# Kernel tuning notes

Hardware: AMD Instinct MI355X
Metric: run time of the kernel (lower is better)

The kernel has to match this reference:

```python
import jax, jax.numpy as jnp
import numpy as np

B, C, H, W = 16, 256, 32, 32
LN_EPS = 1e-5


def setup_inputs() -> dict:
    key = jax.random.key(0)
    ks = jax.random.split(key, 12)
    s = 1.0 / np.sqrt(C)
    x = jax.random.normal(ks[0], (B, C, H, W), dtype=jnp.float32)
    # Linear weights stored as [in, out] (torch stores [out, in]; math is x @ W_in_out + b)
    wq = jax.random.uniform(ks[1], (C, C), jnp.float32, -s, s)
    bq = jax.random.uniform(ks[2], (C,), jnp.float32, -s, s)
    wk = jax.random.uniform(ks[3], (C, C), jnp.float32, -s, s)
    bk = jax.random.uniform(ks[4], (C,), jnp.float32, -s, s)
    wv = jax.random.uniform(ks[5], (C, C), jnp.float32, -s, s)
    bv = jax.random.uniform(ks[6], (C,), jnp.float32, -s, s)
    w1 = jax.random.uniform(ks[7], (C, C), jnp.float32, -s, s)
    b1 = jax.random.uniform(ks[8], (C,), jnp.float32, -s, s)
    w2 = jax.random.uniform(ks[9], (C, C), jnp.float32, -s, s)
    b2 = jax.random.uniform(ks[10], (C,), jnp.float32, -s, s)
    gamma = jnp.ones((C,), jnp.float32)
    beta = jnp.zeros((C,), jnp.float32)
    return {"x": x, "wq": wq, "bq": bq, "wk": wk, "bk": bk, "wv": wv, "bv": bv,
            "w1": w1, "b1": b1, "w2": w2, "b2": b2, "gamma": gamma, "beta": beta}


def reference(x, wq, bq, wk, bk, wv, bv, w1, b1, w2, b2, gamma, beta):
    Bd, Cd, Hd, Wd = x.shape
    t = x.reshape(Bd, Cd, Hd * Wd).transpose(0, 2, 1)  # [B, N, C]
    q = t @ wq + bq
    k = t @ wk + bk
    v = t @ wv + bv
    # matrix[b,i,j] = q[b,i,:] . k[b,j,:]  (no 1/sqrt(d) scaling, as in source)
    m = jnp.einsum('bic,bjc->bij', q, k)
    # softmax over dim=-2 (the query axis i)
    m = jax.nn.softmax(m, axis=-2)
    # att[b,j,c] = sum_i v[b,i,c] * m[b,i,j]  (v^T @ m, then permute)
    att = jnp.einsum('bic,bij->bjc', v, m)  # [B, N, C]
    # MLP (SiLU, hidden = C), dropout p=0 -> identity; DropPath eval -> identity
    att = jax.nn.silu(att @ w1 + b1) @ w2 + b2
    # LayerNorm over channel dim
    mu = jnp.mean(att, axis=-1, keepdims=True)
    var = jnp.var(att, axis=-1, keepdims=True)
    att = (att - mu) * jax.lax.rsqrt(var + LN_EPS) * gamma + beta
    return att.transpose(0, 2, 1).reshape(Bd, Cd, Hd, Wd)
```

## Files before the change

### kernel.cpp

```cpp
#include <hip/hip_runtime.h>

#define BB 16
#define CC 256
#define NN 1024

typedef _Float16 f16;
typedef __attribute__((ext_vector_type(8))) _Float16 half8;
typedef __attribute__((ext_vector_type(4))) float f32x4;

__device__ __forceinline__ half8 ldg8(const f16* p) {
  return *reinterpret_cast<const half8*>(p);
}

__device__ __forceinline__ void gll16(const f16* g, f16* l) {
  __builtin_amdgcn_global_load_lds((const __attribute__((address_space(1))) void*)g,
                                   (__attribute__((address_space(3))) void*)l, 16, 0, 0);
}

#define VMCNT(n) asm volatile("s_waitcnt vmcnt(" #n ")" ::: "memory")
#define BAR() __builtin_amdgcn_s_barrier()

__device__ __forceinline__ void stage32k8(const f16* __restrict__ g, f16* l, int wave, int lane) {
#pragma unroll
  for (int k = 0; k < 4; ++k) {
    int ob = k * 4096 + wave * 512;
    gll16(g + ob + lane * 8, l + ob);
  }
}

struct WP5 {
  const float* s[5];
  f16* d[5];
};

__global__ void __launch_bounds__(256) k_packW(WP5 p) {
  __shared__ float ws[256][17];
  int m = blockIdx.y, ct = blockIdx.x;
  const float* W = p.s[m];
  f16* wp = p.d[m];
  int tid = threadIdx.x;
  int col = tid & 15, cig = tid >> 4;
#pragma unroll
  for (int pg = 0; pg < 16; ++pg) {
    int ci = pg * 16 + cig;
    ws[ci][col] = W[(size_t)ci * 256 + ct * 16 + col];
  }
  __syncthreads();
  int lane = tid & 63, wave = tid >> 6;
  int row16 = lane & 15, quad = lane >> 4;
#pragma unroll
  for (int kk = 0; kk < 2; ++kk) {
    int kc = wave * 2 + kk;
    half8 o;
#pragma unroll
    for (int j = 0; j < 8; ++j) o[j] = (f16)ws[kc * 32 + quad * 8 + j][row16];
    *reinterpret_cast<half8*>(wp + ((size_t)ct * 8 + kc) * 512 + lane * 8) = o;
  }
}

struct QkvSmem {
  union {
    struct { f16 hi[32][264]; f16 lo[32][264]; } ts;
    f16 ex[2][16][264];
    f16 exv[256][40];
  };
};

__global__ void __launch_bounds__(256) k_qkv(const float* __restrict__ x,
    const f16* __restrict__ wqp, const f16* __restrict__ wkp, const f16* __restrict__ wvp,
    const float* __restrict__ bq, const float* __restrict__ bk, const float* __restrict__ bv,
    f16* __restrict__ qp, f16* __restrict__ kp, f16* __restrict__ vp, int b_base) {
  __shared__ QkvSmem sm;
  int bl = blockIdx.x, bg = b_base + bl, n0 = blockIdx.y * 32;
  int tid = threadIdx.x, wave = tid >> 6, lane = tid & 63;
  int row16 = lane & 15, quad = lane >> 4;
  int g = wave >> 1, h = wave & 1;

#pragma unroll
  for (int e = tid; e < 2048; e += 256) {
    int c = e >> 3, n4 = (e & 7) << 2;
    float4 u = *reinterpret_cast<const float4*>(x + (size_t)(bg * CC + c) * NN + n0 + n4);
    float uv[4] = {u.x, u.y, u.z, u.w};
#pragma unroll
    for (int i = 0; i < 4; ++i) {
      f16 hh = (f16)uv[i];
      sm.ts.hi[n4 + i][c] = hh;
      sm.ts.lo[n4 + i][c] = (f16)(uv[i] - (float)hh);
    }
  }
  __syncthreads();

  half8 ah[8], al[8];
#pragma unroll
  for (int kc = 0; kc < 8; ++kc) {
    ah[kc] = *reinterpret_cast<const half8*>(&sm.ts.hi[g * 16 + row16][kc * 32 + quad * 8]);
    al[kc] = *reinterpret_cast<const half8*>(&sm.ts.lo[g * 16 + row16][kc * 32 + quad * 8]);
  }
  __syncthreads();

  const f16* WTs[2]    = {wqp, wkp};
  const float* biases[2] = {bq, bk};
  f16* outs[2]         = {qp, kp};
#pragma unroll
  for (int z = 0; z < 2; ++z) {
    const f16* WT = WTs[z];
    const float* bias = biases[z];
    f16* outp = outs[z];
#pragma unroll
    for (int cp = 0; cp < 2; ++cp) {
      f32x4 acch[4], accl[4];
#pragma unroll
      for (int u = 0; u < 4; ++u) { acch[u] = {0.f,0.f,0.f,0.f}; accl[u] = {0.f,0.f,0.f,0.f}; }
#pragma unroll
      for (int kc = 0; kc < 8; ++kc) {
#pragma unroll
        for (int u = 0; u < 4; ++u) {
          int ct = h * 8 + cp * 4 + u;
          half8 b = ldg8(WT + ((size_t)ct * 8 + kc) * 512 + lane * 8);
          acch[u] = __builtin_amdgcn_mfma_f32_16x16x32_f16(ah[kc], b, acch[u], 0, 0, 0);
          accl[u] = __builtin_amdgcn_mfma_f32_16x16x32_f16(al[kc], b, accl[u], 0, 0, 0);
        }
      }
#pragma unroll
      for (int u = 0; u < 4; ++u) {
        int ct = h * 8 + cp * 4 + u;
        int co = ct * 16 + row16;
        float bb = bias[co];
#pragma unroll
        for (int r = 0; r < 4; ++r)
          sm.ex[g][quad * 4 + r][co] = (f16)(acch[u][r] + accl[u][r] + bb);
      }
    }
    const f16* exr = &sm.ex[g][row16][0];
    size_t fb = ((size_t)bl * 64 + (n0 >> 4) + g) * 8;
#pragma unroll
    for (int k = 0; k < 4; ++k) {
      int kc = h * 4 + k;
      half8 hv = *reinterpret_cast<const half8*>(exr + kc * 32 + quad * 8);
      *reinterpret_cast<half8*>(outp + (fb + kc) * 512 + lane * 8) = hv;
    }
  }
  __syncthreads();

#pragma unroll
  for (int cp = 0; cp < 2; ++cp) {
    f32x4 acch[4], accl[4];
#pragma unroll
    for (int u = 0; u < 4; ++u) { acch[u] = {0.f,0.f,0.f,0.f}; accl[u] = {0.f,0.f,0.f,0.f}; }
#pragma unroll
    for (int kc = 0; kc < 8; ++kc) {
#pragma unroll
      for (int u = 0; u < 4; ++u) {
        int ct = h * 8 + cp * 4 + u;
        half8 b = ldg8(wvp + ((size_t)ct * 8 + kc) * 512 + lane * 8);
        acch[u] = __builtin_amdgcn_mfma_f32_16x16x32_f16(ah[kc], b, acch[u], 0, 0, 0);
        accl[u] = __builtin_amdgcn_mfma_f32_16x16x32_f16(al[kc], b, accl[u], 0, 0, 0);
      }
    }
#pragma unroll
    for (int u = 0; u < 4; ++u) {
      int ct = h * 8 + cp * 4 + u;
      int co = ct * 16 + row16;
      float bb = bv[co];
#pragma unroll
      for (int r = 0; r < 4; ++r)
        sm.exv[co][g * 16 + quad * 4 + r] = (f16)(acch[u][r] + accl[u][r] + bb);
    }
  }
  __syncthreads();
  size_t vb = ((size_t)bl * 32 + blockIdx.y) * 16;
#pragma unroll
  for (int f = 0; f < 4; ++f) {
    int ct = wave * 4 + f;
    half8 o = *reinterpret_cast<const half8*>(&sm.exv[ct * 16 + row16][quad * 8]);
    *reinterpret_cast<half8*>(vp + (vb + ct) * 512 + lane * 8) = o;
  }
}

struct AttnSmem {
  union {
    struct {
      f16 QB[64 * 256];
      f16 VB[64 * 256];
    } s;
    struct {
      float Ocmb[4][16][132];
      f16 ex[4][16][264];
    } e;
  } u;
  f16 P[8][16][40];
  float ml[8][2][16];
  float lnbuf[8][2][16];
};

__global__ void __launch_bounds__(512, 2) k_attn_mlp(
    const f16* __restrict__ qp, const f16* __restrict__ kp, const f16* __restrict__ vp,
    const f16* __restrict__ w1p, const float* __restrict__ b1,
    const f16* __restrict__ w2p, const float* __restrict__ b2,
    const float* __restrict__ gamma, const float* __restrict__ beta,
    float* __restrict__ out, int b_base) {
  __shared__ AttnSmem sm;
  int bl = blockIdx.x, bg = b_base + bl;
  int j0 = blockIdx.y * 64;
  int tid = threadIdx.x, wave = tid >> 6, lane = tid & 63;
  int row16 = lane & 15, quad = lane >> 4;
  int jt_l = wave & 3, p = wave >> 2;
  int jw = j0 + jt_l * 16;

  const f16* kbase = kp + (size_t)bl * NN * CC;
  int jt = (j0 >> 4) + jt_l;
  half8 kf[8];
#pragma unroll
  for (int kc = 0; kc < 8; ++kc)
    kf[kc] = ldg8(kbase + ((size_t)jt * 8 + kc) * 512 + lane * 8);

  const f16* qbase = qp + (size_t)bl * NN * CC;
  const f16* vbase = vp + (size_t)bl * CC * NN;

  stage32k8(qbase, sm.u.s.QB, wave, lane);
  stage32k8(vbase, sm.u.s.VB, wave, lane);
  VMCNT(4);
  BAR();

  f32x4 O[16];
#pragma unroll
  for (int ct = 0; ct < 16; ++ct) O[ct] = {0.f, 0.f, 0.f, 0.f};
  float m_run[4], l_lane[4];
#pragma unroll
  for (int r = 0; r < 4; ++r) { m_run[r] = -1e30f; l_lane[r] = 0.f; }

  const f16* QBp = &sm.u.s.QB[p * 8192];
  const f16* VBp = &sm.u.s.VB[p * 8192];

  for (int it = 0; it < 16; ++it) {
    f32x4 s[2];
#pragma unroll
    for (int f = 0; f < 2; ++f) s[f] = {0.f, 0.f, 0.f, 0.f};
#pragma unroll
    for (int kc = 0; kc < 8; ++kc) {
#pragma unroll
      for (int f = 0; f < 2; ++f) {
        half8 b = *reinterpret_cast<const half8*>(&QBp[(f * 8 + kc) * 512 + lane * 8]);
        s[f] = __builtin_amdgcn_mfma_f32_16x16x32_f16(kf[kc], b, s[f], 0, 0, 0);
      }
    }
    BAR();
    stage32k8(qbase + (size_t)((it + 1) & 15) * 16384, sm.u.s.QB, wave, lane);

    float alpha[4];
#pragma unroll
    for (int r = 0; r < 4; ++r) {
      float mx = fmaxf(s[0][r], s[1][r]);
#pragma unroll
      for (int off = 1; off < 16; off <<= 1) mx = fmaxf(mx, __shfl_xor(mx, off, 64));
      float mnew = fmaxf(m_run[r], mx);
      alpha[r] = __expf(m_run[r] - mnew);
      m_run[r] = mnew;
      float ps = 0.f;
#pragma unroll
      for (int f = 0; f < 2; ++f) {
        float pv = __expf(s[f][r] - mnew);
        ps += pv;
        sm.P[wave][quad * 4 + r][f * 16 + row16] = (f16)pv;
      }
      l_lane[r] = l_lane[r] * alpha[r] + ps;
    }
#pragma unroll
    for (int ct = 0; ct < 16; ++ct)
#pragma unroll
      for (int r = 0; r < 4; ++r) O[ct][r] *= alpha[r];

    VMCNT(4);
    BAR();

    {
      half8 pf = *reinterpret_cast<const half8*>(&sm.P[wave][row16][quad * 8]);
#pragma unroll
      for (int ct = 0; ct < 16; ++ct) {
        half8 vf = *reinterpret_cast<const half8*>(&VBp[ct * 512 + lane * 8]);
        O[ct] = __builtin_amdgcn_mfma_f32_16x16x32_f16(pf, vf, O[ct], 0, 0, 0);
      }
    }
    BAR();
    stage32k8(vbase + (size_t)((it + 1) & 15) * 16384, sm.u.s.VB, wave, lane);
    VMCNT(4);
    BAR();
  }
  VMCNT(0);
  BAR();

#pragma unroll
  for (int r = 0; r < 4; ++r) {
#pragma unroll
    for (int off = 1; off < 16; off <<= 1) l_lane[r] += __shfl_xor(l_lane[r], off, 64);
  }
  if (row16 == 0) {
#pragma unroll
    for (int r = 0; r < 4; ++r) {
      sm.ml[wave][0][quad * 4 + r] = m_run[r];
      sm.ml[wave][1][quad * 4 + r] = l_lane[r];
    }
  }
  BAR();

  int partner = wave ^ 4;
  float aS[4], invL[4];
#pragma unroll
  for (int r = 0; r < 4; ++r) {
    int j = quad * 4 + r;
    float ma = m_run[r], mb = sm.ml[partner][0][j];
    float M = fmaxf(ma, mb);
    float L = l_lane[r] * __expf(ma - M) + sm.ml[partner][1][j] * __expf(mb - M);
    aS[r] = __expf(ma - M);
    invL[r] = 1.f / L;
  }
#pragma unroll
  for (int ct = 0; ct < 16; ++ct)
#pragma unroll
    for (int r = 0; r < 4; ++r) O[ct][r] *= aS[r];

  if (p == 0) {
#pragma unroll
    for (int ct = 0; ct < 8; ++ct)
#pragma unroll
      for (int r = 0; r < 4; ++r)
        sm.u.e.Ocmb[jt_l][quad * 4 + r][ct * 16 + row16] = O[ct][r];
  }
  BAR();
  if (p == 1) {
#pragma unroll
    for (int ct = 0; ct < 8; ++ct)
#pragma unroll
      for (int r = 0; r < 4; ++r) {
        float v = sm.u.e.Ocmb[jt_l][quad * 4 + r][ct * 16 + row16] + O[ct][r];
        sm.u.e.ex[jt_l][quad * 4 + r][ct * 16 + row16] = (f16)(v * invL[r]);
      }
  }
  BAR();
  if (p == 0) {
#pragma unroll
    for (int ct = 8; ct < 16; ++ct)
#pragma unroll
      for (int r = 0; r < 4; ++r)
        sm.u.e.Ocmb[jt_l][quad * 4 + r][(ct - 8) * 16 + row16] = O[ct][r];
  }
  BAR();
  if (p == 1) {
#pragma unroll
    for (int ct = 8; ct < 16; ++ct)
#pragma unroll
      for (int r = 0; r < 4; ++r) {
        float v = sm.u.e.Ocmb[jt_l][quad * 4 + r][(ct - 8) * 16 + row16] + O[ct][r];
        sm.u.e.ex[jt_l][quad * 4 + r][ct * 16 + row16] = (f16)(v * invL[r]);
      }
  }
  BAR();

  half8 af[8];
#pragma unroll
  for (int kc = 0; kc < 8; ++kc)
    af[kc] = *reinterpret_cast<const half8*>(&sm.u.e.ex[jt_l][row16][kc * 32 + quad * 8]);

  f16* ex2 = reinterpret_cast<f16*>(&sm.u.e.Ocmb[0][0][0]);

#pragma unroll
  for (int q8 = 0; q8 < 8; ++q8) {
    int ct = p * 8 + q8;
    f32x4 acc = {0.f, 0.f, 0.f, 0.f};
    const f16* brow = w1p + ((size_t)ct * 8) * 512 + lane * 8;
#pragma unroll
    for (int kc = 0; kc < 8; ++kc)
      acc = __builtin_amdgcn_mfma_f32_16x16x32_f16(af[kc], ldg8(brow + kc * 512), acc, 0, 0, 0);
    int co = ct * 16 + row16;
    float bb = b1[co];
#pragma unroll
    for (int r = 0; r < 4; ++r) {
      float xg = acc[r] + bb;
      float hh = xg / (1.f + __expf(-xg));
      ex2[((size_t)jt_l * 16 + quad * 4 + r) * 264 + co] = (f16)hh;
    }
  }
  BAR();

  half8 hf[8];
#pragma unroll
  for (int kc = 0; kc < 8; ++kc)
    hf[kc] = *reinterpret_cast<const half8*>(&ex2[((size_t)jt_l * 16 + row16) * 264 + kc * 32 + quad * 8]);

  f32x4 acc2[8];
#pragma unroll
  for (int q8 = 0; q8 < 8; ++q8) {
    int ct = p * 8 + q8;
    f32x4 acc = {0.f, 0.f, 0.f, 0.f};
    const f16* brow = w2p + ((size_t)ct * 8) * 512 + lane * 8;
#pragma unroll
    for (int kc = 0; kc < 8; ++kc)
      acc = __builtin_amdgcn_mfma_f32_16x16x32_f16(hf[kc], ldg8(brow + kc * 512), acc, 0, 0, 0);
    float bb = b2[ct * 16 + row16];
#pragma unroll
    for (int r = 0; r < 4; ++r) acc[r] += bb;
    acc2[q8] = acc;
  }

  float sum[4] = {0.f, 0.f, 0.f, 0.f}, ssq[4] = {0.f, 0.f, 0.f, 0.f};
#pragma unroll
  for (int q8 = 0; q8 < 8; ++q8)
#pragma unroll
    for (int r = 0; r < 4; ++r) { float xv = acc2[q8][r]; sum[r] += xv; ssq[r] += xv * xv; }
#pragma unroll
  for (int r = 0; r < 4; ++r) {
#pragma unroll
    for (int off = 1; off < 16; off <<= 1) {
      sum[r] += __shfl_xor(sum[r], off, 64);
      ssq[r] += __shfl_xor(ssq[r], off, 64);
    }
  }
  if (row16 == 0) {
#pragma unroll
    for (int r = 0; r < 4; ++r) {
      sm.lnbuf[wave][0][quad * 4 + r] = sum[r];
      sm.lnbuf[wave][1][quad * 4 + r] = ssq[r];
    }
  }
  BAR();

  float mean[4], rstd[4];
#pragma unroll
  for (int r = 0; r < 4; ++r) {
    int j = quad * 4 + r;
    float s  = sm.lnbuf[wave][0][j] + sm.lnbuf[partner][0][j];
    float sq = sm.lnbuf[wave][1][j] + sm.lnbuf[partner][1][j];
    mean[r] = s * (1.f / 256.f);
    float var = sq * (1.f / 256.f) - mean[r] * mean[r];
    rstd[r] = rsqrtf(var + 1e-5f);
  }

#pragma unroll
  for (int q8 = 0; q8 < 8; ++q8) {
    int col = (p * 8 + q8) * 16 + row16;
    float g = gamma[col], be = beta[col];
    f32x4 v;
#pragma unroll
    for (int r = 0; r < 4; ++r) v[r] = (acc2[q8][r] - mean[r]) * rstd[r] * g + be;
    *reinterpret_cast<f32x4*>(out + (size_t)(bg * CC + col) * NN + jw + quad * 4) = v;
  }
}

extern "C" void kernel_launch(void* const* d_in, const int* in_sizes, int n_in,
                              void* d_out, int out_size, void* d_ws, size_t ws_size,
                              hipStream_t stream) {
  (void)in_sizes; (void)n_in; (void)out_size;
  const float* x     = (const float*)d_in[0];
  const float* wq    = (const float*)d_in[1];
  const float* bq    = (const float*)d_in[2];
  const float* wk    = (const float*)d_in[3];
  const float* bk    = (const float*)d_in[4];
  const float* wv    = (const float*)d_in[5];
  const float* bv    = (const float*)d_in[6];
  const float* w1    = (const float*)d_in[7];
  const float* b1    = (const float*)d_in[8];
  const float* w2    = (const float*)d_in[9];
  const float* b2    = (const float*)d_in[10];
  const float* gamma = (const float*)d_in[11];
  const float* beta  = (const float*)d_in[12];
  float* out = (float*)d_out;

  const size_t WE = 65536;
  const size_t SB = (size_t)NN * CC;
  f16* base = (f16*)d_ws;
  f16* wqp = base + 0 * WE;
  f16* wkp = base + 1 * WE;
  f16* wvp = base + 2 * WE;
  f16* w1p = base + 3 * WE;
  f16* w2p = base + 4 * WE;

  size_t wbytes = 5 * WE * sizeof(f16);
  size_t perb   = 3 * SB * sizeof(f16);
  int nb = (ws_size > wbytes) ? (int)((ws_size - wbytes) / perb) : 1;
  if (nb < 1) nb = 1;
  if (nb > BB) nb = BB;

  f16* qb  = base + 5 * WE;
  f16* kb  = qb + (size_t)nb * SB;
  f16* vTb = kb + (size_t)nb * SB;

  WP5 p;
  p.s[0] = wq; p.s[1] = wk; p.s[2] = wv; p.s[3] = w1; p.s[4] = w2;
  p.d[0] = wqp; p.d[1] = wkp; p.d[2] = wvp; p.d[3] = w1p; p.d[4] = w2p;
  k_packW<<<dim3(16, 5), 256, 0, stream>>>(p);

  for (int b0 = 0; b0 < BB; b0 += nb) {
    int cb = (b0 + nb <= BB) ? nb : (BB - b0);
    k_qkv<<<dim3(cb, 32), 256, 0, stream>>>(x, wqp, wkp, wvp, bq, bk, bv, qb, kb, vTb, b0);
    k_attn_mlp<<<dim3(cb, 16), 512, 0, stream>>>(qb, kb, vTb, w1p, b1, w2p, b2,
                                                 gamma, beta, out, b0);
  }
}
```

Measured before the change: 187.5 us.

## Double-buffer Q/V staging in attention loop and merge combine passes

```diff
diff --git a/kernel.cpp b/kernel.cpp
--- a/kernel.cpp
+++ b/kernel.cpp
@@ -66,7 +66,7 @@
   };
 };
 
-__global__ void __launch_bounds__(256) k_qkv(const float* __restrict__ x,
+__global__ void __launch_bounds__(256, 2) k_qkv(const float* __restrict__ x,
     const f16* __restrict__ wqp, const f16* __restrict__ wkp, const f16* __restrict__ wvp,
     const float* __restrict__ bq, const float* __restrict__ bk, const float* __restrict__ bv,
     f16* __restrict__ qp, f16* __restrict__ kp, f16* __restrict__ vp, int b_base) {
@@ -180,11 +180,11 @@
 struct AttnSmem {
   union {
     struct {
-      f16 QB[64 * 256];
-      f16 VB[64 * 256];
+      f16 QB[2][64 * 256];
+      f16 VB[2][64 * 256];
     } s;
     struct {
-      float Ocmb[4][16][132];
+      float Ocmb[4][16][260];
       f16 ex[4][16][264];
     } e;
   } u;
@@ -217,9 +217,9 @@
   const f16* qbase = qp + (size_t)bl * NN * CC;
   const f16* vbase = vp + (size_t)bl * CC * NN;
 
-  stage32k8(qbase, sm.u.s.QB, wave, lane);
-  stage32k8(vbase, sm.u.s.VB, wave, lane);
-  VMCNT(4);
+  stage32k8(qbase, sm.u.s.QB[0], wave, lane);
+  stage32k8(vbase, sm.u.s.VB[0], wave, lane);
+  VMCNT(0);
   BAR();
 
   f32x4 O[16];
@@ -229,10 +229,14 @@
 #pragma unroll
   for (int r = 0; r < 4; ++r) { m_run[r] = -1e30f; l_lane[r] = 0.f; }
 
-  const f16* QBp = &sm.u.s.QB[p * 8192];
-  const f16* VBp = &sm.u.s.VB[p * 8192];
-
+  int cur = 0;
   for (int it = 0; it < 16; ++it) {
+    const f16* QBp = &sm.u.s.QB[cur][p * 8192];
+    const f16* VBp = &sm.u.s.VB[cur][p * 8192];
+
+    stage32k8(qbase + (size_t)((it + 1) & 15) * 16384, sm.u.s.QB[cur ^ 1], wave, lane);
+    stage32k8(vbase + (size_t)((it + 1) & 15) * 16384, sm.u.s.VB[cur ^ 1], wave, lane);
+
     f32x4 s[2];
 #pragma unroll
     for (int f = 0; f < 2; ++f) s[f] = {0.f, 0.f, 0.f, 0.f};
@@ -244,8 +248,6 @@
         s[f] = __builtin_amdgcn_mfma_f32_16x16x32_f16(kf[kc], b, s[f], 0, 0, 0);
       }
     }
-    BAR();
-    stage32k8(qbase + (size_t)((it + 1) & 15) * 16384, sm.u.s.QB, wave, lane);
 
     float alpha[4];
 #pragma unroll
@@ -270,9 +272,6 @@
 #pragma unroll
       for (int r = 0; r < 4; ++r) O[ct][r] *= alpha[r];
 
-    VMCNT(4);
-    BAR();
-
     {
       half8 pf = *reinterpret_cast<const half8*>(&sm.P[wave][row16][quad * 8]);
 #pragma unroll
@@ -281,13 +280,11 @@
         O[ct] = __builtin_amdgcn_mfma_f32_16x16x32_f16(pf, vf, O[ct], 0, 0, 0);
       }
     }
+
+    VMCNT(0);
     BAR();
-    stage32k8(vbase + (size_t)((it + 1) & 15) * 16384, sm.u.s.VB, wave, lane);
-    VMCNT(4);
-    BAR();
-  }
-  VMCNT(0);
-  BAR();
+    cur ^= 1;
+  }
 
 #pragma unroll
   for (int r = 0; r < 4; ++r) {
@@ -319,38 +316,20 @@
 #pragma unroll
     for (int r = 0; r < 4; ++r) O[ct][r] *= aS[r];
 
-  if (p == 0) {
-#pragma unroll
-    for (int ct = 0; ct < 8; ++ct)
+  if (p == 1) {
+#pragma unroll
+    for (int ct = 0; ct < 16; ++ct)
 #pragma unroll
       for (int r = 0; r < 4; ++r)
         sm.u.e.Ocmb[jt_l][quad * 4 + r][ct * 16 + row16] = O[ct][r];
   }
   BAR();
-  if (p == 1) {
-#pragma unroll
-    for (int ct = 0; ct < 8; ++ct)
+  if (p == 0) {
+#pragma unroll
+    for (int ct = 0; ct < 16; ++ct)
 #pragma unroll
       for (int r = 0; r < 4; ++r) {
         float v = sm.u.e.Ocmb[jt_l][quad * 4 + r][ct * 16 + row16] + O[ct][r];
-        sm.u.e.ex[jt_l][quad * 4 + r][ct * 16 + row16] = (f16)(v * invL[r]);
-      }
-  }
-  BAR();
-  if (p == 0) {
-#pragma unroll
-    for (int ct = 8; ct < 16; ++ct)
-#pragma unroll
-      for (int r = 0; r < 4; ++r)
-        sm.u.e.Ocmb[jt_l][quad * 4 + r][(ct - 8) * 16 + row16] = O[ct][r];
-  }
-  BAR();
-  if (p == 1) {
-#pragma unroll
-    for (int ct = 8; ct < 16; ++ct)
-#pragma unroll
-      for (int r = 0; r < 4; ++r) {
-        float v = sm.u.e.Ocmb[jt_l][quad * 4 + r][(ct - 8) * 16 + row16] + O[ct][r];
         sm.u.e.ex[jt_l][quad * 4 + r][ct * 16 + row16] = (f16)(v * invL[r]);
       }
   }
```

Result: slower. 194.1 us (+3.5%).
